# Kernel optimization log

Hardware: AMD Instinct MI355X
Metric: run time of the kernel (lower is better)

The kernel has to match this reference:

```python
import jax, jax.numpy as jnp
import numpy as np

FACTOR = 5  # ProbAttention factor


def setup_inputs() -> dict:
    key = jax.random.key(0)
    kq, kk, kv = jax.random.split(key, 3)
    B, H, D, L = 4, 8, 64, 4096
    return {
        "queries": jax.random.normal(kq, (B, H, D, L), jnp.float32),
        "keys": jax.random.normal(kk, (B, H, D, L), jnp.float32),
        "values": jax.random.normal(kv, (B, H, D, L), jnp.float32),
        "attn_mask": jnp.zeros((1,), jnp.bool_),  # unused when mask_flag=True (recomputed internally)
    }


def reference(queries, keys, values, attn_mask):
    B, H, D, L_Q = queries.shape  # input layout [B, H, D, L]
    q = jnp.transpose(queries, (0, 1, 3, 2))  # [B,H,L,D]
    k = jnp.transpose(keys, (0, 1, 3, 2))
    v = jnp.transpose(values, (0, 1, 3, 2))
    L_K = k.shape[2]  # true key length (used inside _prob_QK)
    # --- faithful bug from original: L_K/L_V read from queries' LAST dim (=D) ---
    L_K_bug = D
    L_V_bug = D
    U_part = FACTOR * int(np.ceil(np.log(L_K_bug)))
    U_part = U_part if U_part < L_K_bug else L_K_bug  # sample_k
    u = FACTOR * int(np.ceil(np.log(L_Q)))
    u = u if u < L_Q else L_Q  # n_top
    # scaling (bugged denominators for k, v)
    q = q / (np.sqrt(D) * np.sqrt(L_Q))
    k = k / (np.sqrt(D) * np.sqrt(L_K_bug))
    v = v / (np.sqrt(D) * np.sqrt(L_V_bug))

    # ---- _prob_QK: sampled QK, top-u query selection ----
    skey = jax.random.key(42)  # fixed key: deterministic stand-in for torch.randint
    index_sample = jax.random.randint(skey, (L_Q, U_part), 0, L_K)  # [L_Q, U_part]
    K_sample = k[:, :, index_sample, :]  # [B,H,L_Q,U_part,D]
    Q_K_sample = jnp.einsum('bhld,bhlsd->bhls', q, K_sample)  # [B,H,L_Q,U_part]
    M = Q_K_sample.max(-1) - Q_K_sample.sum(-1) / L_K  # sparsity measure, real L_K here
    _, M_top = jax.lax.top_k(M, u)  # [B,H,u] (order irrelevant: distinct scatter targets)
    Q_reduce = jnp.take_along_axis(q, M_top[..., None], axis=2)  # [B,H,u,D]
    scores = jnp.einsum('bhud,bhkd->bhuk', Q_reduce, k)  # [B,H,u,L_K]

    scale = 1.0 / (np.sqrt(D) * np.sqrt(L_Q))  # self.scale is None
    scores = scores * scale

    # ---- initial context (mask_flag=True -> causal cumsum) ----
    context = jnp.cumsum(v, axis=2)  # [B,H,L_Q,D]

    # ---- ProbMask + update ----
    causal = jnp.triu(jnp.ones((L_Q, L_K), jnp.bool_), 1)  # [L_Q, L_K]
    indicator = causal[M_top]  # [B,H,u,L_K]
    scores = jnp.where(indicator, -jnp.inf, scores)
    attn = jax.nn.softmax(scores, axis=-1)
    upd = jnp.einsum('bhuk,bhkd->bhud', attn, v)  # [B,H,u,D]
    bi = jnp.arange(B)[:, None, None]
    hi = jnp.arange(H)[None, :, None]
    context = context.at[bi, hi, M_top].set(upd)

    out = jnp.transpose(context, (0, 1, 3, 2)).reshape(queries.shape)
    return out
```

## Files before the change

### kernel.cpp

```cpp
#include <hip/hip_runtime.h>
#include <cstdint>

constexpr int B_ = 4, H_ = 8, D_ = 64, L_ = 4096;
constexpr int BH = B_ * H_;
constexpr int U_PART = 25;
constexpr int TOPU = 45;
constexpr int CHUNK = 128;
constexpr int NCH = L_ / CHUNK;
constexpr int PSTRIDE = 68;

#define JAX_THREEFRY_PARTITIONABLE 1

__host__ __device__ inline void tf2x32(uint32_t k0, uint32_t k1,
                                       uint32_t x0, uint32_t x1,
                                       uint32_t& y0, uint32_t& y1) {
  const uint32_t ks2 = k0 ^ k1 ^ 0x1BD11BDAu;
  uint32_t v0 = x0 + k0, v1 = x1 + k1;
#define RND(r) { v0 += v1; v1 = (v1 << (r)) | (v1 >> (32 - (r))); v1 ^= v0; }
  RND(13) RND(15) RND(26) RND(6)
  v0 += k1; v1 += ks2 + 1u;
  RND(17) RND(29) RND(16) RND(24)
  v0 += ks2; v1 += k0 + 2u;
  RND(13) RND(15) RND(26) RND(6)
  v0 += k0; v1 += k1 + 3u;
  RND(17) RND(29) RND(16) RND(24)
  v0 += k1; v1 += ks2 + 4u;
  RND(13) RND(15) RND(26) RND(6)
  v0 += ks2; v1 += k0 + 5u;
#undef RND
  y0 = v0; y1 = v1;
}

__global__ __launch_bounds__(256) void prep_kernel(
    const float* __restrict__ k, float* __restrict__ kt,
    int* __restrict__ idx, uint32_t k2a, uint32_t k2b) {
  const int bh = blockIdx.y;
  const int t = threadIdx.x;
#if JAX_THREEFRY_PARTITIONABLE
  {
    const int bid = bh * 64 + blockIdx.x;
    if (t < 50) {
      uint32_t y0, y1;
      const uint32_t i = (uint32_t)(bid * 50 + t);
      tf2x32(k2a, k2b, 0u, i, y0, y1);
      idx[bid * 50 + t] = (int)((y0 ^ y1) & 4095u);
    }
  }
#else
  {
    const int bid = bh * 64 + blockIdx.x;
    const int half = (L_ * U_PART) / 2;
    if (t < 25) {
      uint32_t y0, y1;
      const int j = bid * 25 + t;
      tf2x32(k2a, k2b, (uint32_t)j, (uint32_t)(j + half), y0, y1);
      idx[j] = (int)(y0 & 4095u);
      idx[j + half] = (int)(y1 & 4095u);
    }
  }
#endif
  const int l0 = blockIdx.x * 64;
  __shared__ float tile[64][65];
  const float* s = k + (size_t)bh * D_ * L_ + l0;
  float* d = kt + (size_t)bh * L_ * D_;
  const int rhi = t >> 4, rlo = t & 15;
#pragma unroll
  for (int i = 0; i < 4; i++) {
    const int dd = i * 16 + rhi;
    float4 x = *(const float4*)&s[(size_t)dd * L_ + 4 * rlo];
    tile[dd][4 * rlo + 0] = x.x * (1.0f / 64.0f);
    tile[dd][4 * rlo + 1] = x.y * (1.0f / 64.0f);
    tile[dd][4 * rlo + 2] = x.z * (1.0f / 64.0f);
    tile[dd][4 * rlo + 3] = x.w * (1.0f / 64.0f);
  }
  __syncthreads();
#pragma unroll
  for (int i = 0; i < 4; i++) {
    const int ll = i * 16 + rhi;
    float4 o;
    o.x = tile[4 * rlo + 0][ll];
    o.y = tile[4 * rlo + 1][ll];
    o.z = tile[4 * rlo + 2][ll];
    o.w = tile[4 * rlo + 3][ll];
    *(float4*)&d[(size_t)(l0 + ll) * D_ + 4 * rlo] = o;
  }
}

__device__ __forceinline__ float dpp_bcast_add16(float x) {
  int xi;
  xi = __builtin_amdgcn_mov_dpp(__float_as_int(x), 0x140, 0xF, 0xF, true);
  x += __int_as_float(xi);
  xi = __builtin_amdgcn_mov_dpp(__float_as_int(x), 0x141, 0xF, 0xF, true);
  x += __int_as_float(xi);
  xi = __builtin_amdgcn_mov_dpp(__float_as_int(x), 0x4E, 0xF, 0xF, true);
  x += __int_as_float(xi);
  xi = __builtin_amdgcn_mov_dpp(__float_as_int(x), 0xB1, 0xF, 0xF, true);
  x += __int_as_float(xi);
  return x;
}

__global__ __launch_bounds__(1024) void m_kernel(const float* __restrict__ qraw,
                                                 const float* __restrict__ kt,
                                                 const int* __restrict__ idx,
                                                 float* __restrict__ M) {
  const int t = threadIdx.x;
  const int xcd = blockIdx.x & 7;
  const int slot = blockIdx.x >> 3;
  const int bh = xcd * 4 + (slot >> 6);
  const int l0 = (slot & 63) * 64;
  const float* ktb = kt + (size_t)bh * L_ * D_;
  __shared__ float qs[64][65];
  {
    const float* s = qraw + (size_t)bh * D_ * L_ + l0;
    const int w = t >> 6, lane = t & 63;
#pragma unroll
    for (int j = 0; j < 4; j++) {
      const int d = j * 16 + w;
      qs[lane][d] = s[(size_t)d * L_ + lane] * (1.0f / 512.0f);
    }
  }
  __syncthreads();
  const int grp = t >> 4, gl = t & 15;
  const int l = l0 + grp;
  const float4 ql = *(const float4*)&qs[grp][4 * gl];
  const int* ip = idx + (size_t)l * U_PART;
  float mx = -INFINITY, sm = 0.0f;
#pragma unroll 5
  for (int s2 = 0; s2 < U_PART; s2++) {
    const int ki = ip[s2];
    float4 kk = *(const float4*)(ktb + (size_t)ki * D_ + gl * 4);
    float p = ql.x * kk.x + ql.y * kk.y + ql.z * kk.z + ql.w * kk.w;
    p = dpp_bcast_add16(p);
    mx = fmaxf(mx, p);
    sm += p;
  }
  if (gl == 0) M[bh * L_ + l] = mx - sm * (1.0f / 4096.0f);
}

__global__ __launch_bounds__(256) void topk_cumsum_kernel(
    const float* __restrict__ M, const float* __restrict__ qraw,
    const float* __restrict__ vraw,
    int* __restrict__ ssel_g, float* __restrict__ qsel,
    float* __restrict__ out) {
  const int bid = blockIdx.x;
  const int t = threadIdx.x;
  if (bid >= BH) {
    const int row = bid - BH;
    const float* src = vraw + (size_t)row * L_;
    float* dst = out + (size_t)row * L_;
    float vals[16];
    const float4* s4 = (const float4*)(src + t * 16);
#pragma unroll
    for (int i = 0; i < 4; i++) {
      float4 x = s4[i];
      vals[4 * i + 0] = x.x; vals[4 * i + 1] = x.y;
      vals[4 * i + 2] = x.z; vals[4 * i + 3] = x.w;
    }
    float run = 0.0f;
#pragma unroll
    for (int i = 0; i < 16; i++) { run += vals[i] * (1.0f / 64.0f); vals[i] = run; }
    float x = run;
#pragma unroll
    for (int off = 1; off < 64; off <<= 1) {
      float y = __shfl_up(x, off, 64);
      if ((t & 63) >= off) x += y;
    }
    __shared__ float wtot[4];
    if ((t & 63) == 63) wtot[t >> 6] = x;
    __syncthreads();
    float woff = 0.0f;
    for (int w = 0; w < (t >> 6); w++) woff += wtot[w];
    const float excl = x - run + woff;
#pragma unroll
    for (int i = 0; i < 16; i++) vals[i] += excl;
    float4* d4 = (float4*)(dst + t * 16);
#pragma unroll
    for (int i = 0; i < 4; i++)
      d4[i] = make_float4(vals[4 * i], vals[4 * i + 1], vals[4 * i + 2], vals[4 * i + 3]);
    return;
  }
  const int bh = bid;
  const int w = t >> 6, lane = t & 63;
  const float* Mb = M + (size_t)bh * L_;
  const int base = w * 1024 + lane;
  uint32_t v[16];
#pragma unroll
  for (int j = 0; j < 16; j++) {
    uint32_t b = __float_as_uint(Mb[base + j * 64]);
    v[j] = b ^ ((b & 0x80000000u) ? 0xFFFFFFFFu : 0x80000000u);
  }
  __shared__ unsigned long long red[4];
  __shared__ int picks[TOPU];
  __shared__ int ssorted[TOPU];
  for (int it = 0; it < TOPU; it++) {
    unsigned long long best = 0ull;
#pragma unroll
    for (int j = 0; j < 16; j++) {
      unsigned long long key = ((unsigned long long)v[j] << 32)
                             | (uint32_t)(L_ - 1 - (base + j * 64));
      best = (key > best) ? key : best;
    }
#pragma unroll
    for (int off = 32; off; off >>= 1) {
      unsigned long long o = __shfl_xor(best, off, 64);
      best = (o > best) ? o : best;
    }
    if (lane == 0) red[w] = best;
    __syncthreads();
    unsigned long long g = red[0];
    if (red[1] > g) g = red[1];
    if (red[2] > g) g = red[2];
    if (red[3] > g) g = red[3];
    const int bi = L_ - 1 - (int)(g & 0xFFFFFFFFu);
    if (t == 0) picks[it] = bi;
    if ((bi >> 10) == w && (bi & 63) == lane) {
      const int slot = (bi >> 6) & 15;
#pragma unroll
      for (int j = 0; j < 16; j++) if (slot == j) v[j] = 0u;
    }
    __syncthreads();
  }
  if (t < TOPU) {
    int my = picks[t];
    int rank = 0;
    for (int j = 0; j < TOPU; j++) rank += (picks[j] > my);
    ssorted[rank] = my;
  }
  __syncthreads();
  if (t < TOPU) ssel_g[bh * TOPU + t] = ssorted[t];
  const float* qb = qraw + (size_t)bh * D_ * L_;
  for (int e = t; e < TOPU * 64; e += 256) {
    const int r = e >> 6, d = e & 63;
    qsel[((size_t)bh * TOPU + r) * 64 + e % 64] =
        qb[(size_t)d * L_ + ssorted[r]] * (1.0f / 512.0f);
  }
}

__global__ __launch_bounds__(256) void update_partial(const float* __restrict__ qsel,
                                                      const float* __restrict__ kraw,
                                                      const float* __restrict__ vraw,
                                                      const int* __restrict__ ssel_g,
                                                      float* __restrict__ part) {
  const int xcd = blockIdx.x & 7;
  const int slot = blockIdx.x >> 3;
  const int bh = xcd * 4 + (slot >> 4);
  const int ch0 = slot & 15;
  const int t = threadIdx.x;
  const int w = t >> 6, lane = t & 63;
  const int kl = lane & 15, rg = lane >> 4;

  __shared__ float kv[CHUNK * 64];
  __shared__ float qs[48 * 68];
  __shared__ float eS[48 * 132];
  __shared__ int ssel[48];

  if (t < 48) ssel[t] = (t < TOPU) ? ssel_g[bh * TOPU + t] : -1;
  __syncthreads();

#pragma unroll
  for (int j = 0; j < 3; j++) {
    int it = t + 256 * j;
    int rr = it >> 4, dc = it & 15;
    float4 qv = make_float4(0.f, 0.f, 0.f, 0.f);
    if (rr < TOPU) qv = *(const float4*)&qsel[((size_t)bh * TOPU + rr) * 64 + 4 * dc];
    *(float4*)&qs[rr * 68 + 4 * dc] = qv;
  }

  for (int pass = 0; pass < 2; pass++) {
    const int ch = pass ? (31 - ch0) : ch0;
    const int k0 = ch * CHUNK;
    int lo = 0, hi = TOPU;
    while (lo < hi) { int mid = (lo + hi) >> 1; if (ssel[mid] >= k0) lo = mid + 1; else hi = mid; }
    const int nact = lo;
    if (nact == 0) continue;

    __syncthreads();
    const float* kb = kraw + (size_t)bh * D_ * L_ + k0;
#pragma unroll
    for (int j = 0; j < 8; j++) {
      int e4 = 4 * (t + 256 * j);
      int d = e4 >> 7, key = e4 & 127;
      *(float4*)&kv[e4] = *(const float4*)&kb[(size_t)d * L_ + key];
    }
    __syncthreads();

    const int wr0 = 12 * w;
    if (wr0 < nact) {
      float s[3][8];
#pragma unroll
      for (int j = 0; j < 3; j++)
#pragma unroll
        for (int x = 0; x < 8; x++) s[j][x] = 0.f;
#pragma unroll 8
      for (int d = 0; d < 64; d++) {
        float4 ka = *(const float4*)&kv[d * 128 + 4 * kl];
        float4 kb2 = *(const float4*)&kv[d * 128 + 64 + 4 * kl];
#pragma unroll
        for (int j = 0; j < 3; j++) {
          float qd = qs[(wr0 + 3 * rg + j) * 68 + d];
          s[j][0] += qd * ka.x;  s[j][1] += qd * ka.y;
          s[j][2] += qd * ka.z;  s[j][3] += qd * ka.w;
          s[j][4] += qd * kb2.x; s[j][5] += qd * kb2.y;
          s[j][6] += qd * kb2.z; s[j][7] += qd * kb2.w;
        }
      }
#pragma unroll
      for (int j = 0; j < 3; j++) {
        const int R = wr0 + 3 * rg + j;
        const int sel = ssel[R];
        float mx = -INFINITY;
#pragma unroll
        for (int x = 0; x < 8; x++) {
          int kg = k0 + 4 * kl + (x < 4 ? x : 60 + x);
          s[j][x] *= (1.0f / 32768.0f);
          if (kg > sel) s[j][x] = -INFINITY;
          mx = fmaxf(mx, s[j][x]);
        }
        mx = fmaxf(mx, __shfl_xor(mx, 1, 64));
        mx = fmaxf(mx, __shfl_xor(mx, 2, 64));
        mx = fmaxf(mx, __shfl_xor(mx, 4, 64));
        mx = fmaxf(mx, __shfl_xor(mx, 8, 64));
        float e[8], sm = 0.f;
#pragma unroll
        for (int x = 0; x < 8; x++) { e[x] = expf(s[j][x] - mx); sm += e[x]; }
        sm += __shfl_xor(sm, 1, 64);
        sm += __shfl_xor(sm, 2, 64);
        sm += __shfl_xor(sm, 4, 64);
        sm += __shfl_xor(sm, 8, 64);
        *(float4*)&eS[R * 132 + 4 * kl] = make_float4(e[0], e[1], e[2], e[3]);
        *(float4*)&eS[R * 132 + 64 + 4 * kl] = make_float4(e[4], e[5], e[6], e[7]);
        if (kl == 0 && R < nact) {
          float* p = part + ((size_t)(bh * TOPU + R) * NCH + ch) * PSTRIDE;
          p[64] = mx; p[65] = sm;
        }
      }
    }
    __syncthreads();
    const float* vb = vraw + (size_t)bh * D_ * L_ + k0;
#pragma unroll
    for (int j = 0; j < 8; j++) {
      int e4 = 4 * (t + 256 * j);
      int d = e4 >> 7, kq = (e4 & 127) >> 2;
      float4 vv = *(const float4*)&vb[(size_t)d * L_ + 4 * kq];
      *(float4*)&kv[d * 128 + ((kq ^ (d & 31)) << 2)] = vv;
    }
    __syncthreads();
    if (wr0 < nact) {
      float acc[3][4];
#pragma unroll
      for (int j = 0; j < 3; j++)
#pragma unroll
        for (int x = 0; x < 4; x++) acc[j][x] = 0.f;
      const int dbase = 4 * kl;
#pragma unroll 4
      for (int kb = 0; kb < 32; kb++) {
        float4 ev[3];
#pragma unroll
        for (int j = 0; j < 3; j++)
          ev[j] = *(const float4*)&eS[(wr0 + 3 * rg + j) * 132 + 4 * kb];
#pragma unroll
        for (int x = 0; x < 4; x++) {
          const int dx = dbase + x;
          float4 vv = *(const float4*)&kv[dx * 128 + ((kb ^ (dx & 31)) << 2)];
#pragma unroll
          for (int j = 0; j < 3; j++) {
            acc[j][x] += ev[j].x * vv.x + ev[j].y * vv.y
                       + ev[j].z * vv.z + ev[j].w * vv.w;
          }
        }
      }
#pragma unroll
      for (int j = 0; j < 3; j++) {
        const int R = wr0 + 3 * rg + j;
        if (R < nact) {
          float* p = part + ((size_t)(bh * TOPU + R) * NCH + ch) * PSTRIDE;
          float4 o = make_float4(acc[j][0] * (1.0f / 64.0f), acc[j][1] * (1.0f / 64.0f),
                                 acc[j][2] * (1.0f / 64.0f), acc[j][3] * (1.0f / 64.0f));
          *(float4*)&p[4 * kl] = o;
        }
      }
    }
  }
}

__global__ __launch_bounds__(256) void update_combine(const float* __restrict__ part,
                                                      const int* __restrict__ ssel_g,
                                                      float* __restrict__ out) {
  const int row = blockIdx.x * 4 + (threadIdx.x >> 6);
  if (row >= BH * TOPU) return;
  const int bh = row / TOPU;
  const int sel = ssel_g[row];
  const int d = threadIdx.x & 63;
  const int nv = sel / CHUNK + 1;
  const float* p = part + (size_t)row * NCH * PSTRIDE;

  float m = -INFINITY;
  for (int c = 0; c < nv; c++) m = fmaxf(m, p[c * PSTRIDE + 64]);

  float num = 0.0f, den = 0.0f;
  for (int c = 0; c < nv; c++) {
    float mc = p[c * PSTRIDE + 64];
    float wgt = expf(mc - m);
    num += wgt * p[c * PSTRIDE + d];
    den += wgt * p[c * PSTRIDE + 65];
  }
  out[((size_t)bh * D_ + d) * L_ + sel] = num / den;
}

extern "C" void kernel_launch(void* const* d_in, const int* in_sizes, int n_in,
                              void* d_out, int out_size, void* d_ws, size_t ws_size,
                              hipStream_t stream) {
  const float* q = (const float*)d_in[0];
  const float* k = (const float*)d_in[1];
  const float* v = (const float*)d_in[2];
  float* out = (float*)d_out;

  const size_t NT = (size_t)BH * L_ * D_;
  float* kt = (float*)d_ws;
  float* M  = kt + NT;
  int* idx  = (int*)(M + (size_t)BH * L_);
  int* ssel = idx + L_ * U_PART;
  float* qsel = (float*)(ssel + BH * TOPU);
  float* part = qsel + (size_t)BH * TOPU * 64;

  uint32_t k2a, k2b;
#if JAX_THREEFRY_PARTITIONABLE
  tf2x32(0u, 42u, 0u, 1u, k2a, k2b);
#else
  uint32_t a0, a1, b0, b1;
  tf2x32(0u, 42u, 0u, 2u, a0, a1);
  tf2x32(0u, 42u, 1u, 3u, b0, b1);
  k2a = a1; k2b = b1;
#endif

  prep_kernel<<<dim3(L_ / 64, BH), 256, 0, stream>>>(k, kt, idx, k2a, k2b);
  m_kernel<<<BH * 64, 1024, 0, stream>>>(q, kt, idx, M);
  topk_cumsum_kernel<<<BH + BH * D_, 256, 0, stream>>>(M, q, v, ssel, qsel, out);
  update_partial<<<BH * 16, 256, 0, stream>>>(qsel, k, v, ssel, part);
  update_combine<<<(BH * TOPU + 3) / 4, 256, 0, stream>>>(part, ssel, out);
}
```

Before: 149.3 us.

## Replace K transpose with LDS-resident K chunks and sorted sample indices

Drops the pass that writes a transposed, scaled copy of K to global memory. Instead, each block stages a 512-key chunk of K in a swizzled 128KB LDS buffer and sweeps all queries of its head, using per-query sorted sample indices to binary-search which samples fall in the chunk. Each chunk writes partial max and sum values, which the top-k kernel combines into the sparsity score. The cost is that queries are re-read once per chunk (8 times per head), there is one 1024-thread block per CU with a syncthreads every batch, and a new sorting kernel is added.

Result: slower. 279.4 us (+87.1%).

```diff
diff --git a/kernel.cpp b/kernel.cpp
--- a/kernel.cpp
+++ b/kernel.cpp
@@ -8,6 +8,8 @@
 constexpr int CHUNK = 128;
 constexpr int NCH = L_ / CHUNK;
 constexpr int PSTRIDE = 68;
+constexpr int KCH = 512;
+constexpr int NKCH = L_ / KCH;
 
 #define JAX_THREEFRY_PARTITIONABLE 1
 
@@ -31,59 +33,41 @@
   y0 = v0; y1 = v1;
 }
 
-__global__ __launch_bounds__(256) void prep_kernel(
-    const float* __restrict__ k, float* __restrict__ kt,
-    int* __restrict__ idx, uint32_t k2a, uint32_t k2b) {
-  const int bh = blockIdx.y;
-  const int t = threadIdx.x;
+__global__ __launch_bounds__(256) void threefry_sort_kernel(int* __restrict__ sidx,
+                                                            uint32_t k2a, uint32_t k2b) {
+  const int l = blockIdx.x * 256 + threadIdx.x;
+  if (l >= L_) return;
+  int a[U_PART];
 #if JAX_THREEFRY_PARTITIONABLE
-  {
-    const int bid = bh * 64 + blockIdx.x;
-    if (t < 50) {
-      uint32_t y0, y1;
-      const uint32_t i = (uint32_t)(bid * 50 + t);
-      tf2x32(k2a, k2b, 0u, i, y0, y1);
-      idx[bid * 50 + t] = (int)((y0 ^ y1) & 4095u);
-    }
+#pragma unroll
+  for (int s = 0; s < U_PART; s++) {
+    uint32_t y0, y1;
+    tf2x32(k2a, k2b, 0u, (uint32_t)(l * U_PART + s), y0, y1);
+    a[s] = (int)((y0 ^ y1) & 4095u);
   }
 #else
-  {
-    const int bid = bh * 64 + blockIdx.x;
-    const int half = (L_ * U_PART) / 2;
-    if (t < 25) {
-      uint32_t y0, y1;
-      const int j = bid * 25 + t;
-      tf2x32(k2a, k2b, (uint32_t)j, (uint32_t)(j + half), y0, y1);
-      idx[j] = (int)(y0 & 4095u);
-      idx[j + half] = (int)(y1 & 4095u);
-    }
+  const int half = (L_ * U_PART) / 2;
+#pragma unroll
+  for (int s = 0; s < U_PART; s++) {
+    const int i = l * U_PART + s;
+    uint32_t y0, y1;
+    if (i < half) { tf2x32(k2a, k2b, (uint32_t)i, (uint32_t)(i + half), y0, y1); a[s] = (int)(y0 & 4095u); }
+    else          { tf2x32(k2a, k2b, (uint32_t)(i - half), (uint32_t)i, y0, y1); a[s] = (int)(y1 & 4095u); }
   }
 #endif
-  const int l0 = blockIdx.x * 64;
-  __shared__ float tile[64][65];
-  const float* s = k + (size_t)bh * D_ * L_ + l0;
-  float* d = kt + (size_t)bh * L_ * D_;
-  const int rhi = t >> 4, rlo = t & 15;
-#pragma unroll
-  for (int i = 0; i < 4; i++) {
-    const int dd = i * 16 + rhi;
-    float4 x = *(const float4*)&s[(size_t)dd * L_ + 4 * rlo];
-    tile[dd][4 * rlo + 0] = x.x * (1.0f / 64.0f);
-    tile[dd][4 * rlo + 1] = x.y * (1.0f / 64.0f);
-    tile[dd][4 * rlo + 2] = x.z * (1.0f / 64.0f);
-    tile[dd][4 * rlo + 3] = x.w * (1.0f / 64.0f);
-  }
-  __syncthreads();
-#pragma unroll
-  for (int i = 0; i < 4; i++) {
-    const int ll = i * 16 + rhi;
-    float4 o;
-    o.x = tile[4 * rlo + 0][ll];
-    o.y = tile[4 * rlo + 1][ll];
-    o.z = tile[4 * rlo + 2][ll];
-    o.w = tile[4 * rlo + 3][ll];
-    *(float4*)&d[(size_t)(l0 + ll) * D_ + 4 * rlo] = o;
-  }
+#pragma unroll
+  for (int r = 0; r < U_PART; r++) {
+#pragma unroll
+    for (int p = 0; p + 1 < U_PART; p += 2) {
+      const int pp = p + (r & 1);
+      if (pp + 1 < U_PART) {
+        int x = a[pp], y = a[pp + 1];
+        a[pp] = min(x, y); a[pp + 1] = max(x, y);
+      }
+    }
+  }
+#pragma unroll
+  for (int s = 0; s < U_PART; s++) sidx[l * U_PART + s] = a[s];
 }
 
 __device__ __forceinline__ float dpp_bcast_add16(float x) {
@@ -99,47 +83,92 @@
   return x;
 }
 
-__global__ __launch_bounds__(1024) void m_kernel(const float* __restrict__ qraw,
-                                                 const float* __restrict__ kt,
-                                                 const int* __restrict__ idx,
-                                                 float* __restrict__ M) {
+__global__ __launch_bounds__(1024) void m_chunk_kernel(const float* __restrict__ qraw,
+                                                       const float* __restrict__ kraw,
+                                                       const int* __restrict__ sidx,
+                                                       float* __restrict__ partM,
+                                                       float* __restrict__ partS) {
+  const int bid = blockIdx.x;
+  const int xcd = bid & 7;
+  const int slot = bid >> 3;
+  const int bh = xcd * 4 + (slot & 3);
+  const int c = slot >> 2;
+  const int kbase = c * KCH;
   const int t = threadIdx.x;
-  const int xcd = blockIdx.x & 7;
-  const int slot = blockIdx.x >> 3;
-  const int bh = xcd * 4 + (slot >> 6);
-  const int l0 = (slot & 63) * 64;
-  const float* ktb = kt + (size_t)bh * L_ * D_;
+  const int w = t >> 6, lane = t & 63;
+
+  __shared__ float kc[KCH * 64];
   __shared__ float qs[64][65];
+  __shared__ int sidxS[64 * U_PART];
+
   {
-    const float* s = qraw + (size_t)bh * D_ * L_ + l0;
-    const int w = t >> 6, lane = t & 63;
+    const float* kb = kraw + (size_t)bh * D_ * L_ + kbase;
 #pragma unroll
     for (int j = 0; j < 4; j++) {
       const int d = j * 16 + w;
-      qs[lane][d] = s[(size_t)d * L_ + lane] * (1.0f / 512.0f);
-    }
-  }
-  __syncthreads();
-  const int grp = t >> 4, gl = t & 15;
-  const int l = l0 + grp;
-  const float4 ql = *(const float4*)&qs[grp][4 * gl];
-  const int* ip = idx + (size_t)l * U_PART;
-  float mx = -INFINITY, sm = 0.0f;
-#pragma unroll 5
-  for (int s2 = 0; s2 < U_PART; s2++) {
-    const int ki = ip[s2];
-    float4 kk = *(const float4*)(ktb + (size_t)ki * D_ + gl * 4);
-    float p = ql.x * kk.x + ql.y * kk.y + ql.z * kk.z + ql.w * kk.w;
-    p = dpp_bcast_add16(p);
-    mx = fmaxf(mx, p);
-    sm += p;
-  }
-  if (gl == 0) M[bh * L_ + l] = mx - sm * (1.0f / 4096.0f);
+      const int dq = d >> 2, dr = d & 3;
+#pragma unroll
+      for (int jj = 0; jj < 2; jj++) {
+        const int key0 = jj * 256 + lane * 4;
+        float4 x = *(const float4*)&kb[(size_t)d * L_ + key0];
+        float vv[4] = {x.x, x.y, x.z, x.w};
+#pragma unroll
+        for (int i = 0; i < 4; i++) {
+          const int key = key0 + i;
+          const int g = key * 16 + (dq ^ ((key >> 2) & 15));
+          kc[4 * g + dr] = vv[i];
+        }
+      }
+    }
+  }
+
+  for (int batch = 0; batch < 64; batch++) {
+    const int l0 = batch * 64;
+    __syncthreads();
+    {
+      const float* s = qraw + (size_t)bh * D_ * L_ + l0;
+#pragma unroll
+      for (int j = 0; j < 4; j++) {
+        const int d = j * 16 + w;
+        qs[lane][d] = s[(size_t)d * L_ + lane] * (1.0f / 512.0f);
+      }
+      const int* ib = sidx + (size_t)l0 * U_PART;
+#pragma unroll
+      for (int j = 0; j < 2; j++) {
+        const int i = t + 1024 * j;
+        if (i < 64 * U_PART) sidxS[i] = ib[i];
+      }
+    }
+    __syncthreads();
+    const int grp = t >> 4, gl = t & 15;
+    const float4 ql = *(const float4*)&qs[grp][4 * gl];
+    const int* sp = sidxS + grp * U_PART;
+    int lo = 0, hi = U_PART;
+    while (lo < hi) { int mid = (lo + hi) >> 1; if (sp[mid] < kbase) lo = mid + 1; else hi = mid; }
+    int a2 = lo, b2 = U_PART;
+    while (a2 < b2) { int mid = (a2 + b2) >> 1; if (sp[mid] < kbase + KCH) a2 = mid + 1; else b2 = mid; }
+    const int hi2 = a2;
+    float mx = -INFINITY, sm = 0.0f;
+    for (int j = lo; j < hi2; j++) {
+      const int ki = sp[j] - kbase;
+      const int g = ki * 16 + (gl ^ ((ki >> 2) & 15));
+      const float4 kk = *(const float4*)&kc[4 * g];
+      float p = ql.x * kk.x + ql.y * kk.y + ql.z * kk.z + ql.w * kk.w;
+      p = dpp_bcast_add16(p);
+      mx = fmaxf(mx, p);
+      sm += p;
+    }
+    if (gl == 0) {
+      const size_t o = (size_t)(bh * NKCH + c) * L_ + l0 + grp;
+      partM[o] = mx;
+      partS[o] = sm;
+    }
+  }
 }
 
 __global__ __launch_bounds__(256) void topk_cumsum_kernel(
-    const float* __restrict__ M, const float* __restrict__ qraw,
-    const float* __restrict__ vraw,
+    const float* __restrict__ partM, const float* __restrict__ partS,
+    const float* __restrict__ qraw, const float* __restrict__ vraw,
     int* __restrict__ ssel_g, float* __restrict__ qsel,
     float* __restrict__ out) {
   const int bid = blockIdx.x;
@@ -181,12 +210,21 @@
   }
   const int bh = bid;
   const int w = t >> 6, lane = t & 63;
-  const float* Mb = M + (size_t)bh * L_;
+  const float* pMb = partM + (size_t)bh * NKCH * L_;
+  const float* pSb = partS + (size_t)bh * NKCH * L_;
   const int base = w * 1024 + lane;
   uint32_t v[16];
 #pragma unroll
   for (int j = 0; j < 16; j++) {
-    uint32_t b = __float_as_uint(Mb[base + j * 64]);
+    const int e = base + j * 64;
+    float mxv = -INFINITY, smv = 0.0f;
+#pragma unroll
+    for (int cc = 0; cc < NKCH; cc++) {
+      mxv = fmaxf(mxv, pMb[(size_t)cc * L_ + e]);
+      smv += pSb[(size_t)cc * L_ + e];
+    }
+    const float Mv = mxv - smv * (1.0f / 4096.0f);
+    uint32_t b = __float_as_uint(Mv);
     v[j] = b ^ ((b & 0x80000000u) ? 0xFFFFFFFFu : 0x80000000u);
   }
   __shared__ unsigned long long red[4];
@@ -415,13 +453,12 @@
   const float* v = (const float*)d_in[2];
   float* out = (float*)d_out;
 
-  const size_t NT = (size_t)BH * L_ * D_;
-  float* kt = (float*)d_ws;
-  float* M  = kt + NT;
-  int* idx  = (int*)(M + (size_t)BH * L_);
-  int* ssel = idx + L_ * U_PART;
+  int* sidx = (int*)d_ws;
+  int* ssel = sidx + L_ * U_PART;
   float* qsel = (float*)(ssel + BH * TOPU);
-  float* part = qsel + (size_t)BH * TOPU * 64;
+  float* partM = qsel + (size_t)BH * TOPU * 64;
+  float* partS = partM + (size_t)BH * NKCH * L_;
+  float* part  = partS + (size_t)BH * NKCH * L_;
 
   uint32_t k2a, k2b;
 #if JAX_THREEFRY_PARTITIONABLE
@@ -433,9 +470,9 @@
   k2a = a1; k2b = b1;
 #endif
 
-  prep_kernel<<<dim3(L_ / 64, BH), 256, 0, stream>>>(k, kt, idx, k2a, k2b);
-  m_kernel<<<BH * 64, 1024, 0, stream>>>(q, kt, idx, M);
-  topk_cumsum_kernel<<<BH + BH * D_, 256, 0, stream>>>(M, q, v, ssel, qsel, out);
+  threefry_sort_kernel<<<(L_ + 255) / 256, 256, 0, stream>>>(sidx, k2a, k2b);
+  m_chunk_kernel<<<256, 1024, 0, stream>>>(q, k, sidx, partM, partS);
+  topk_cumsum_kernel<<<BH + BH * D_, 256, 0, stream>>>(partM, partS, q, v, ssel, qsel, out);
   update_partial<<<BH * 16, 256, 0, stream>>>(qsel, k, v, ssel, part);
   update_combine<<<(BH * TOPU + 3) / 4, 256, 0, stream>>>(part, ssel, out);
 }
```
